# Performance work log

Measured on AMD Instinct MI355X. Metric: run time of the kernel, lower is better.

Reference implementation:

```python
import jax, jax.numpy as jnp
import numpy as np

T, B, IN, H, OUT = 2048, 64, 32, 512, 32


def setup_inputs() -> dict:
    key = jax.random.key(0)
    ks = jax.random.split(key, 7)
    s = 1.0 / np.sqrt(H)
    return {
        "inputs": jax.random.normal(ks[0], (T, B, IN), dtype=jnp.float32),
        "h0": jnp.zeros((B, H), dtype=jnp.float32),
        "c0": jnp.zeros((B, H), dtype=jnp.float32),
        "W_ih": jax.random.uniform(ks[1], (4 * H, IN), minval=-s, maxval=s, dtype=jnp.float32),
        "W_hh": jax.random.uniform(ks[2], (4 * H, H), minval=-s, maxval=s, dtype=jnp.float32),
        "b_ih": jax.random.uniform(ks[3], (4 * H,), minval=-s, maxval=s, dtype=jnp.float32),
        "b_hh": jax.random.uniform(ks[4], (4 * H,), minval=-s, maxval=s, dtype=jnp.float32),
        "W_out": jax.random.uniform(ks[5], (OUT, H), minval=-s, maxval=s, dtype=jnp.float32),
        "b_out": jax.random.uniform(ks[6], (OUT,), minval=-s, maxval=s, dtype=jnp.float32),
    }


def reference(inputs, h0, c0, W_ih, W_hh, b_ih, b_hh, W_out, b_out):
    Hh = h0.shape[-1]
    # Precompute input projections for all timesteps: [T, B, 4H]
    x_proj = jnp.einsum('tbi,gi->tbg', inputs, W_ih) + b_ih + b_hh

    def step(carry, xp):
        h, c = carry
        gates = xp + h @ W_hh.T  # [B, 4H]
        i, f, g, o = jnp.split(gates, 4, axis=-1)  # torch LSTMCell gate order
        i = jax.nn.sigmoid(i)
        f = jax.nn.sigmoid(f)
        g = jnp.tanh(g)
        o = jax.nn.sigmoid(o)
        c_new = f * c + i * g
        h_new = o * jnp.tanh(c_new)
        return (h_new, c_new), h_new

    (h_T, c_T), h_all = jax.lax.scan(step, (h0, c0), x_proj)
    outputs = jnp.einsum('tbh,oh->tbo', h_all, W_out) + b_out  # [T, B, OUT]
    return outputs, (h_T, c_T)
```

## Files before the change

### kernel.cpp

```cpp
#include <hip/hip_runtime.h>

#define TT 2048
#define BB 64
#define INF 32
#define HH 512
#define OO 32

typedef __attribute__((ext_vector_type(8))) short bf16x8;
typedef __attribute__((ext_vector_type(4))) float f32x4;

__device__ __forceinline__ float sigm(float x) {
  return 1.f / (1.f + __expf(-x));
}
__device__ __forceinline__ float tanh_(float x) {
  float e = __expf(2.f * x);
  return 1.f - 2.f / (1.f + e);
}
__device__ __forceinline__ unsigned short f2bf(float f) {
  unsigned u = __float_as_uint(f);
  u = (u + 0x7FFFu + ((u >> 16) & 1u)) >> 16;
  return (unsigned short)u;
}
__device__ __forceinline__ float bf2f(unsigned short s) {
  return __uint_as_float(((unsigned)s) << 16);
}

#define COH_LOAD4(dst, ptr)                                                  \
  asm volatile("global_load_dwordx4 %0, %1, off sc0 sc1"                     \
               : "=v"(dst) : "v"(ptr))

#define SPIN_LIMIT 20000

#define HSTR 528

__global__ __launch_bounds__(512, 2)
void lstm_fused(const float* __restrict__ X,
                const float* __restrict__ h0,
                const float* __restrict__ c0,
                const float* __restrict__ Wih,
                const float* __restrict__ Whh,
                const float* __restrict__ bih,
                const float* __restrict__ bhh,
                const float* __restrict__ Wout,
                const float* __restrict__ bout,
                float* __restrict__ outp,
                float* __restrict__ hT,
                float* __restrict__ cT,
                unsigned short* __restrict__ hring,
                int* __restrict__ flags)
{
  const int tid    = threadIdx.x;
  const int rg     = tid >> 6;
  const int lane   = tid & 63;
  const int bg     = blockIdx.x & 7;
  const int sl     = blockIdx.x >> 3;
  const int bglob0 = bg << 3;

  __shared__ __align__(16) unsigned short hlds[8 * HSTR];

  const bool mwave = (rg < 4);

  bf16x8 aW[16], aX;
  float biasf[4];
  if (mwave) {
    const int ri = lane & 15;
    const int arow = ((ri & 3) << 9) + (sl << 4) + (rg << 2) + (ri >> 2);
    const float* wb = Whh + (size_t)arow * HH + ((lane >> 4) << 3);
#pragma unroll
    for (int kt = 0; kt < 16; ++kt) {
      float4 a = ((const float4*)(wb + kt * 32))[0];
      float4 b = ((const float4*)(wb + kt * 32))[1];
      bf16x8 f;
      f[0] = (short)f2bf(a.x); f[1] = (short)f2bf(a.y);
      f[2] = (short)f2bf(a.z); f[3] = (short)f2bf(a.w);
      f[4] = (short)f2bf(b.x); f[5] = (short)f2bf(b.y);
      f[6] = (short)f2bf(b.z); f[7] = (short)f2bf(b.w);
      aW[kt] = f;
    }
    const float* wi = Wih + (size_t)arow * INF + ((lane >> 4) << 3);
    float4 a = ((const float4*)wi)[0];
    float4 b = ((const float4*)wi)[1];
    aX[0] = (short)f2bf(a.x); aX[1] = (short)f2bf(a.y);
    aX[2] = (short)f2bf(a.z); aX[3] = (short)f2bf(a.w);
    aX[4] = (short)f2bf(b.x); aX[5] = (short)f2bf(b.y);
    aX[6] = (short)f2bf(b.z); aX[7] = (short)f2bf(b.w);
#pragma unroll
    for (int r = 0; r < 4; ++r) {
      int grow = (r << 9) + (sl << 4) + (rg << 2) + (lane >> 4);
      biasf[r] = bih[grow] + bhh[grow];
    }
  }
  float wout[8];
  {
    const float4* wp = (const float4*)(Wout + sl * HH + (lane << 3));
    float4 a = wp[0], b4 = wp[1];
    wout[0] = a.x;  wout[1] = a.y;  wout[2] = a.z;  wout[3] = a.w;
    wout[4] = b4.x; wout[5] = b4.y; wout[6] = b4.z; wout[7] = b4.w;
  }
  const float bo = bout[sl];

  const bool owner = mwave && ((lane & 15) < 8);
  const int ob = lane & 7;
  const int ojj = (rg << 2) + (lane >> 4);
  const int hoff_owner = (bglob0 + ob) * HH + (sl << 4) + ojj;
  float cst = owner ? c0[hoff_owner] : 0.f;

  const int lb = tid >> 6, lg = tid & 63;
  int* myflags = flags + (bg << 5);

  for (int t = 0; t < TT; ++t) {
    float4 xva, xvb;
    if (mwave) {
      const float* xr = X + (size_t)t * BB * INF + (bglob0 + (lane & 7)) * INF
                        + ((lane >> 4) << 3);
      xva = ((const float4*)xr)[0];
      xvb = ((const float4*)xr)[1];
    }

    if (t > 0 && rg == 0) {
      int f = __hip_atomic_load(&myflags[lane & 31], __ATOMIC_RELAXED,
                                __HIP_MEMORY_SCOPE_AGENT);
      int guard = 0;
      while (__any(f < t)) {
        if (++guard > SPIN_LIMIT) break;
        __builtin_amdgcn_s_sleep(1);
        f = __hip_atomic_load(&myflags[lane & 31], __ATOMIC_RELAXED,
                              __HIP_MEMORY_SCOPE_AGENT);
      }
    }
    __syncthreads();

    if (t == 0) {
      const float* hp = h0 + (size_t)(bglob0 + lb) * HH + (lg << 3);
      float4 a = ((const float4*)hp)[0];
      float4 b = ((const float4*)hp)[1];
      unsigned d0 = (unsigned)f2bf(a.x) | ((unsigned)f2bf(a.y) << 16);
      unsigned d1 = (unsigned)f2bf(a.z) | ((unsigned)f2bf(a.w) << 16);
      unsigned d2 = (unsigned)f2bf(b.x) | ((unsigned)f2bf(b.y) << 16);
      unsigned d3 = (unsigned)f2bf(b.z) | ((unsigned)f2bf(b.w) << 16);
      *(int4*)(hlds + lb * HSTR + (lg << 3)) = make_int4(d0, d1, d2, d3);
    } else {
      const unsigned short* hsrc = hring + (size_t)((t - 1) & 1) * BB * HH
                                   + (size_t)(bglob0 + lb) * HH + (lg << 3);
      int4 hv;
      COH_LOAD4(hv, hsrc);
      asm volatile("s_waitcnt vmcnt(0)" ::: "memory");
      __builtin_amdgcn_sched_barrier(0);
      *(int4*)(hlds + lb * HSTR + (lg << 3)) = hv;
    }
    __syncthreads();

    float o0 = 0.f, o1 = 0.f;
    if (mwave) {
      f32x4 acc = {0.f, 0.f, 0.f, 0.f};
      bf16x8 bx;
      bx[0] = (short)f2bf(xva.x); bx[1] = (short)f2bf(xva.y);
      bx[2] = (short)f2bf(xva.z); bx[3] = (short)f2bf(xva.w);
      bx[4] = (short)f2bf(xvb.x); bx[5] = (short)f2bf(xvb.y);
      bx[6] = (short)f2bf(xvb.z); bx[7] = (short)f2bf(xvb.w);
      acc = __builtin_amdgcn_mfma_f32_16x16x32_bf16(aX, bx, acc, 0, 0, 0);
      const unsigned short* hb = hlds + (lane & 7) * HSTR + ((lane >> 4) << 3);
#pragma unroll
      for (int kt = 0; kt < 16; ++kt) {
        bf16x8 bf = *(const bf16x8*)(hb + kt * 32);
        acc = __builtin_amdgcn_mfma_f32_16x16x32_bf16(aW[kt], bf, acc, 0, 0, 0);
      }
      float i_ = sigm(acc[0] + biasf[0]);
      float f_ = sigm(acc[1] + biasf[1]);
      float g_ = tanh_(acc[2] + biasf[2]);
      float o_ = sigm(acc[3] + biasf[3]);
      float cnew = __fmaf_rn(f_, cst, i_ * g_);
      float hv = o_ * tanh_(cnew);
      if (owner) cst = cnew;
      float hv2 = __shfl(hv, (lane + 16) & 63, 64);
      if (owner && ((lane >> 4) & 1) == 0) {
        unsigned pk = (unsigned)f2bf(hv) | ((unsigned)f2bf(hv2) << 16);
        unsigned* slot32 = (unsigned*)(hring + (size_t)(t & 1) * BB * HH);
        __hip_atomic_store(
            &slot32[((bglob0 + ob) << 8) + (sl << 3) + (rg << 1) + (lane >> 5)],
            pk, __ATOMIC_RELAXED, __HIP_MEMORY_SCOPE_AGENT);
      }
      if (owner && t == TT - 1) { hT[hoff_owner] = hv; cT[hoff_owner] = cst; }
    } else {
      const int wb2 = (rg - 4) << 1;
      const bf16x8 ha = *(const bf16x8*)(hlds + wb2 * HSTR + (lane << 3));
      const bf16x8 hc = *(const bf16x8*)(hlds + (wb2 + 1) * HSTR + (lane << 3));
#pragma unroll
      for (int j = 0; j < 8; ++j) {
        o0 = __fmaf_rn(bf2f((unsigned short)ha[j]), wout[j], o0);
        o1 = __fmaf_rn(bf2f((unsigned short)hc[j]), wout[j], o1);
      }
#pragma unroll
      for (int s = 32; s >= 1; s >>= 1) {
        o0 += __shfl_xor(o0, s, 64);
        o1 += __shfl_xor(o1, s, 64);
      }
    }
    __syncthreads();
    if (tid == 0)
      __hip_atomic_store(&myflags[sl], t + 1, __ATOMIC_RELAXED,
                         __HIP_MEMORY_SCOPE_AGENT);
    if (!mwave && t > 0 && lane == 0) {
      const int wb2 = (rg - 4) << 1;
      outp[(size_t)(t - 1) * BB * OO + (bglob0 + wb2) * OO + sl] = o0 + bo;
      outp[(size_t)(t - 1) * BB * OO + (bglob0 + wb2 + 1) * OO + sl] = o1 + bo;
    }
  }

  if (rg == 0) {
    int f = __hip_atomic_load(&myflags[lane & 31], __ATOMIC_RELAXED,
                              __HIP_MEMORY_SCOPE_AGENT);
    int guard = 0;
    while (__any(f < TT)) {
      if (++guard > SPIN_LIMIT) break;
      __builtin_amdgcn_s_sleep(1);
      f = __hip_atomic_load(&myflags[lane & 31], __ATOMIC_RELAXED,
                            __HIP_MEMORY_SCOPE_AGENT);
    }
  }
  __syncthreads();
  {
    const unsigned short* hb = hring + (size_t)((TT - 1) & 1) * BB * HH
                               + (size_t)(bglob0 + rg) * HH + (lane << 3);
    int4 p;
    COH_LOAD4(p, hb);
    asm volatile("s_waitcnt vmcnt(0)" ::: "memory");
    __builtin_amdgcn_sched_barrier(0);
    float oacc =
        __uint_as_float(((unsigned)p.x) << 16)        * wout[0] +
        __uint_as_float(((unsigned)p.x) & 0xFFFF0000u) * wout[1] +
        __uint_as_float(((unsigned)p.y) << 16)        * wout[2] +
        __uint_as_float(((unsigned)p.y) & 0xFFFF0000u) * wout[3] +
        __uint_as_float(((unsigned)p.z) << 16)        * wout[4] +
        __uint_as_float(((unsigned)p.z) & 0xFFFF0000u) * wout[5] +
        __uint_as_float(((unsigned)p.w) << 16)        * wout[6] +
        __uint_as_float(((unsigned)p.w) & 0xFFFF0000u) * wout[7];
#pragma unroll
    for (int s = 32; s >= 1; s >>= 1) oacc += __shfl_xor(oacc, s, 64);
    if (lane == 0)
      outp[(size_t)(TT - 1) * BB * OO + (bglob0 + rg) * OO + sl] = oacc + bo;
  }
}

extern "C" void kernel_launch(void* const* d_in, const int* in_sizes, int n_in,
                              void* d_out, int out_size, void* d_ws, size_t ws_size,
                              hipStream_t stream) {
  const float* X    = (const float*)d_in[0];
  const float* h0   = (const float*)d_in[1];
  const float* c0   = (const float*)d_in[2];
  const float* Wih  = (const float*)d_in[3];
  const float* Whh  = (const float*)d_in[4];
  const float* bih  = (const float*)d_in[5];
  const float* bhh  = (const float*)d_in[6];
  const float* Wout = (const float*)d_in[7];
  const float* bout = (const float*)d_in[8];

  float* outp = (float*)d_out;
  float* hT   = outp + (size_t)TT * BB * OO;
  float* cT   = hT + (size_t)BB * HH;

  unsigned short* hring = (unsigned short*)d_ws;
  int* flags = (int*)((char*)d_ws + (size_t)2 * BB * HH * sizeof(unsigned short));

  hipMemsetAsync(flags, 0, 8 * 32 * sizeof(int), stream);

  lstm_fused<<<dim3(256), dim3(512), 0, stream>>>(
      X, h0, c0, Wih, Whh, bih, bhh, Wout, bout, outp, hT, cT, hring, flags);
}
```

Measured before the change: 4.122 ms.

## Poll flags in every wave, drop barriers, split MFMA accumulator chain

Every wave now spins on the cross-block step flags itself instead of wave 0 polling and then releasing the block with a __syncthreads, which removes one block barrier per timestep and another at the end. The input bf16 conversion is moved ahead of the wait so it overlaps with the polling. The recurrent MFMA chain is split across two accumulators to shorten the dependent chain. The cost is more global atomic polling traffic from all waves, plus a slightly different summation order.

```diff
diff --git a/kernel.cpp b/kernel.cpp
--- a/kernel.cpp
+++ b/kernel.cpp
@@ -109,15 +109,19 @@
   int* myflags = flags + (bg << 5);
 
   for (int t = 0; t < TT; ++t) {
-    float4 xva, xvb;
+    bf16x8 bx;
     if (mwave) {
       const float* xr = X + (size_t)t * BB * INF + (bglob0 + (lane & 7)) * INF
                         + ((lane >> 4) << 3);
-      xva = ((const float4*)xr)[0];
-      xvb = ((const float4*)xr)[1];
-    }
-
-    if (t > 0 && rg == 0) {
+      float4 xva = ((const float4*)xr)[0];
+      float4 xvb = ((const float4*)xr)[1];
+      bx[0] = (short)f2bf(xva.x); bx[1] = (short)f2bf(xva.y);
+      bx[2] = (short)f2bf(xva.z); bx[3] = (short)f2bf(xva.w);
+      bx[4] = (short)f2bf(xvb.x); bx[5] = (short)f2bf(xvb.y);
+      bx[6] = (short)f2bf(xvb.z); bx[7] = (short)f2bf(xvb.w);
+    }
+
+    if (t > 0) {
       int f = __hip_atomic_load(&myflags[lane & 31], __ATOMIC_RELAXED,
                                 __HIP_MEMORY_SCOPE_AGENT);
       int guard = 0;
@@ -128,7 +132,6 @@
                               __HIP_MEMORY_SCOPE_AGENT);
       }
     }
-    __syncthreads();
 
     if (t == 0) {
       const float* hp = h0 + (size_t)(bglob0 + lb) * HH + (lg << 3);
@@ -152,23 +155,21 @@
 
     float o0 = 0.f, o1 = 0.f;
     if (mwave) {
-      f32x4 acc = {0.f, 0.f, 0.f, 0.f};
-      bf16x8 bx;
-      bx[0] = (short)f2bf(xva.x); bx[1] = (short)f2bf(xva.y);
-      bx[2] = (short)f2bf(xva.z); bx[3] = (short)f2bf(xva.w);
-      bx[4] = (short)f2bf(xvb.x); bx[5] = (short)f2bf(xvb.y);
-      bx[6] = (short)f2bf(xvb.z); bx[7] = (short)f2bf(xvb.w);
-      acc = __builtin_amdgcn_mfma_f32_16x16x32_bf16(aX, bx, acc, 0, 0, 0);
+      f32x4 acc0 = {0.f, 0.f, 0.f, 0.f};
+      f32x4 acc1 = {0.f, 0.f, 0.f, 0.f};
+      acc0 = __builtin_amdgcn_mfma_f32_16x16x32_bf16(aX, bx, acc0, 0, 0, 0);
       const unsigned short* hb = hlds + (lane & 7) * HSTR + ((lane >> 4) << 3);
 #pragma unroll
-      for (int kt = 0; kt < 16; ++kt) {
-        bf16x8 bf = *(const bf16x8*)(hb + kt * 32);
-        acc = __builtin_amdgcn_mfma_f32_16x16x32_bf16(aW[kt], bf, acc, 0, 0, 0);
-      }
-      float i_ = sigm(acc[0] + biasf[0]);
-      float f_ = sigm(acc[1] + biasf[1]);
-      float g_ = tanh_(acc[2] + biasf[2]);
-      float o_ = sigm(acc[3] + biasf[3]);
+      for (int kt = 0; kt < 16; kt += 2) {
+        bf16x8 bf0 = *(const bf16x8*)(hb + kt * 32);
+        bf16x8 bf1 = *(const bf16x8*)(hb + (kt + 1) * 32);
+        acc0 = __builtin_amdgcn_mfma_f32_16x16x32_bf16(aW[kt], bf0, acc0, 0, 0, 0);
+        acc1 = __builtin_amdgcn_mfma_f32_16x16x32_bf16(aW[kt + 1], bf1, acc1, 0, 0, 0);
+      }
+      float i_ = sigm(acc0[0] + acc1[0] + biasf[0]);
+      float f_ = sigm(acc0[1] + acc1[1] + biasf[1]);
+      float g_ = tanh_(acc0[2] + acc1[2] + biasf[2]);
+      float o_ = sigm(acc0[3] + acc1[3] + biasf[3]);
       float cnew = __fmaf_rn(f_, cst, i_ * g_);
       float hv = o_ * tanh_(cnew);
       if (owner) cst = cnew;
@@ -207,7 +208,7 @@
     }
   }
 
-  if (rg == 0) {
+  {
     int f = __hip_atomic_load(&myflags[lane & 31], __ATOMIC_RELAXED,
                               __HIP_MEMORY_SCOPE_AGENT);
     int guard = 0;
@@ -218,7 +219,6 @@
                             __HIP_MEMORY_SCOPE_AGENT);
     }
   }
-  __syncthreads();
   {
     const unsigned short* hb = hring + (size_t)((TT - 1) & 1) * BB * HH
                                + (size_t)(bglob0 + rg) * HH + (lane << 3);
```

After: 3.961 ms. 3.9% less time.
